# Performance work log

Hardware: AMD Instinct MI355X
Metric: run time of the kernel (lower is better)

## Reference

```python
import jax, jax.numpy as jnp
import numpy as np


def setup_inputs() -> dict:
    key = jax.random.key(0)
    B, T = 16384, 768
    inputs = jax.random.normal(key, (B, T, 2), dtype=jnp.float32)
    p = {"capacitance_x": 0.4, "capacitance_y": 0.4}
    for d in ["ax", "by", "xx", "xy", "yx", "yy"]:
        p[f"conductance_{d}"] = 0.001
        p[f"mean_{d}"] = 0.3
        p[f"std_{d}"] = 3.0
        p[f"pot_{d}"] = -1.0 if d in ("xy", "yx") else 1.0
    params = {k: jnp.full((1,), v, dtype=jnp.float32) for k, v in p.items()}
    return {"inputs": inputs, **params}


def reference(inputs, capacitance_x, capacitance_y,
              conductance_ax, mean_ax, std_ax, pot_ax,
              conductance_by, mean_by, std_by, pot_by,
              conductance_xx, mean_xx, std_xx, pot_xx,
              conductance_xy, mean_xy, std_xy, pot_xy,
              conductance_yx, mean_yx, std_yx, pot_yx,
              conductance_yy, mean_yy, std_yy, pot_yy):
    # inputs: [B, T, 2]; scan over T with carried state [B, 2]
    def syn(g, s, m, p, pre, post):
        # conductance * sigmoid(std*(pre-mean)) * (pot - post)
        return g * jax.nn.sigmoid(s * (pre - m)) * (p - post)

    def step(carry, inp):
        x, y = carry[:, :1], carry[:, 1:]          # [B,1] each
        a, b = inp[:, :1], inp[:, 1:]              # [B,1] each
        ix = (syn(conductance_ax, std_ax, mean_ax, pot_ax, a, x)
              + syn(conductance_xx, std_xx, mean_xx, pot_xx, x, x)
              + syn(conductance_yx, std_yx, mean_yx, pot_yx, y, x))
        iy = (syn(conductance_by, std_by, mean_by, pot_by, b, y)
              + syn(conductance_yy, std_yy, mean_yy, pot_yy, y, y)
              + syn(conductance_xy, std_xy, mean_xy, pot_xy, x, y))
        x = x + ix / capacitance_x
        y = y + iy / capacitance_y
        return jnp.concatenate([x, y], axis=-1), x

    B = inputs.shape[0]
    init = jnp.zeros((B, 2), dtype=inputs.dtype)
    _, ys = jax.lax.scan(step, init, jnp.swapaxes(inputs, 0, 1))  # ys: [T,B,1]
    return jnp.swapaxes(ys, 0, 1)  # [B,T,1]
```

## Files before the change

kernel.cpp:

```cpp
#include <hip/hip_runtime.h>

#define T_LEN 768
#define TC 64
#define NCH (T_LEN / TC)
#define RPB 32
#define RS  66
#define OS  66

struct Params { const float* p[27]; };

__device__ __forceinline__ float ex2(float x){ float r; asm("v_exp_f32 %0, %1":"=v"(r):"v"(x)); return r; }
__device__ __forceinline__ float frcp(float x){ return __builtin_amdgcn_rcpf(x); }
__device__ __forceinline__ float dpp_xor1(float x){
    return __int_as_float(__builtin_amdgcn_mov_dpp(__float_as_int(x),0xB1,0xF,0xF,true));
}
__device__ __forceinline__ float psig(float v, float k, float c){
    return frcp(1.0f + ex2(__builtin_fmaf(-k, v, c)));
}
__device__ __forceinline__ void wave_barrier(){
    asm volatile("s_waitcnt lgkmcnt(0)" ::: "memory");
    __builtin_amdgcn_s_barrier();
}

__global__ __launch_bounds__(192, 1) void cell_kernel(Params P, float* __restrict__ out) {
    __shared__ float r1buf[2][TC][RS];
    __shared__ float lds_o[2][TC][OS];

    const int tid = (int)threadIdx.x;
    const int r0  = (int)blockIdx.x * RPB;
    const int wv  = tid >> 6;
    const int l   = tid & 63;

    const float* __restrict__ inp = P.p[0];
    const float capx = P.p[1][0], capy = P.p[2][0];
    const float g_ax = P.p[3][0],  m_ax = P.p[4][0],  s_ax = P.p[5][0],  q_ax = P.p[6][0];
    const float g_by = P.p[7][0],  m_by = P.p[8][0],  s_by = P.p[9][0],  q_by = P.p[10][0];
    const float g_xx = P.p[11][0], m_xx = P.p[12][0], s_xx = P.p[13][0], q_xx = P.p[14][0];
    const float g_xy = P.p[15][0], m_xy = P.p[16][0], s_xy = P.p[17][0], q_xy = P.p[18][0];
    const float g_yx = P.p[19][0], m_yx = P.p[20][0], s_yx = P.p[21][0], q_yx = P.p[22][0];
    const float g_yy = P.p[23][0], m_yy = P.p[24][0], s_yy = P.p[25][0], q_yy = P.p[26][0];

    const float icx = 1.0f / capx, icy = 1.0f / capy;
    const float L2E  = 1.44269504088896340736f;
    const float LN2  = 0.69314718056f;
    const float mLN2 = -0.69314718056f;
    const float mHLN2 = -0.34657359028f;

    const float k1x = s_ax * L2E, c1x = k1x * m_ax;
    const float k1y = s_by * L2E, c1y = k1y * m_by;

    const bool share = (s_yx == s_yy) && (m_yx == m_yy) &&
                       (s_xy == s_xx) && (m_xy == m_xx) &&
                       (s_xx != 0.0f) && (s_yy != 0.0f) &&
                       (g_xx != 0.0f) && (g_yy != 0.0f);

    const float k2xp = s_xx * L2E, c2xp = k2xp * m_xx;
    const float G2xp = g_xx * icx;
    const float A2xp = g_xx * q_xx * icx;
    const float R2xp = __builtin_fmaf(G2xp, c2xp, -k2xp * A2xp);
    const float cv1 = share ? 1.0f / (G2xp * k2xp) : 1.0f;
    const float cv0 = share ? (c2xp / k2xp - R2xp * (1.0f / (G2xp * k2xp))) : 0.0f;

    const float4* __restrict__ in4 = (const float4*)inp;

    if (wv != 0) {
        const int p = wv - 1;
        float4 pinA[8], pinB[8];

        auto LOADP = [&](float4 (&pin)[8], int c) {
            #pragma unroll
            for (int k = 0; k < 8; ++k) { int idx = l + 64*(p*8 + k);
                int r_ = idx >> 5, q = idx & 31;
                pin[k] = in4[(size_t)(r0 + r_) * 384 + c * 32 + q]; }
        };
        auto SIGW = [&](float4 (&pin)[8], int buf) {
            #pragma unroll
            for (int k = 0; k < 8; ++k) { int idx = l + 64*(p*8 + k);
                int r_ = idx >> 5, q = idx & 31;
                float2 w0, w1;
                w0.x = psig(pin[k].x, k1x, c1x);
                w0.y = psig(pin[k].y, k1y, c1y);
                w1.x = psig(pin[k].z, k1x, c1x);
                w1.y = psig(pin[k].w, k1y, c1y);
                *(float2*)&r1buf[buf][2*q]    [2*r_] = w0;
                *(float2*)&r1buf[buf][2*q + 1][2*r_] = w1; }
        };
        auto DRAIN = [&](int c) {
            const int buf = c & 1;
            #pragma unroll
            for (int k = 0; k < 4; ++k) { int f = l + 64*(p*4 + k);
                int r_ = f >> 4, pq = f & 15;
                float4 o;
                o.x = __builtin_fmaf(lds_o[buf][4*pq + 0][2*r_], cv1, cv0);
                o.y = __builtin_fmaf(lds_o[buf][4*pq + 1][2*r_], cv1, cv0);
                o.z = __builtin_fmaf(lds_o[buf][4*pq + 2][2*r_], cv1, cv0);
                o.w = __builtin_fmaf(lds_o[buf][4*pq + 3][2*r_], cv1, cv0);
                *(float4*)&out[(size_t)(r0 + r_) * T_LEN + c * TC + 4*pq] = o; }
        };

        LOADP(pinA, 0);
        LOADP(pinB, 1);
        SIGW(pinA, 0);
        wave_barrier();
        for (int c = 0; c < NCH; ++c) {
            if (c + 2 < NCH) { if ((c & 1) == 0) LOADP(pinA, c + 2);
                               else              LOADP(pinB, c + 2); }
            if (c >= 1) DRAIN(c - 1);
            if (c + 1 < NCH) {
                if ((c & 1) == 0) SIGW(pinB, (c + 1) & 1);
                else              SIGW(pinA, (c + 1) & 1);
            }
            wave_barrier();
        }
        DRAIN(NCH - 1);
    } else {
        __builtin_amdgcn_s_setprio(1);

        const bool isX = (l & 1) == 0;
        const float k2r = (isX ? s_xx : s_yy) * L2E;
        const float c2r = k2r * (isX ? m_xx : m_yy);
        const float k3r = (isX ? s_xy : s_yx) * L2E;
        const float c3r = k3r * (isX ? m_xy : m_yx);
        const float icr = isX ? icx : icy;
        const float A1r = (isX ? g_ax * q_ax : g_by * q_by) * icr, G1r = (isX ? g_ax : g_by) * icr;
        const float A2r = (isX ? g_xx * q_xx : g_yy * q_yy) * icr, G2r = (isX ? g_xx : g_yy) * icr;
        const float A3r = (isX ? g_yx * q_yx : g_xy * q_xy) * icr, G3r = (isX ? g_yx : g_xy) * icr;

        const float R1 = __builtin_fmaf(G1r, c2r, -k2r * A1r);
        const float R2 = __builtin_fmaf(G2r, c2r, -k2r * A2r);
        const float R3 = __builtin_fmaf(G3r, c2r, -k2r * A3r);
        const float mG1 = -G1r, mG2 = -G2r, mG3 = -G3r;
        const float inv_mG2 = 1.0f / mG2;

        float h1 = __builtin_fmaf(mG1, c2r, R1);
        float h2 = __builtin_fmaf(mG2, c2r, R2);
        float h3 = __builtin_fmaf(mG3, c2r, R3);
        float v = 0.0f;

        wave_barrier();
        for (int c = 0; c < NCH; ++c) {
            const int buf = c & 1;
            float rr[TC];
            #pragma unroll
            for (int t = 0; t < TC; ++t) rr[t] = r1buf[buf][t][l];

            if (share) {
                float Wr  = (h2 - R2) * inv_mG2;
                float E   = ex2(Wr);
                float sg  = frcp(1.0f + E);
                float t1  = __builtin_fmaf(-sg, sg, sg);
                float cfac = mLN2 * t1;
                float w2  = __builtin_fmaf(LN2, sg, mHLN2);
                float hd2 = cfac * w2;
                float dl2p = 0.0f;
                float p1 = rr[0] * h1;
                #pragma unroll
                for (int t = 0; t < TC; ++t) {
                    float rp   = dpp_xor1(sg);
                    float s2mW = __builtin_fmaf(sg, h2, p1);
                    float dl   = __builtin_fmaf(rp, h3, s2mW);
                    float inner = __builtin_fmaf(hd2, dl2p, sg);
                    float sgn  = __builtin_fmaf(cfac, dl, inner);
                    dl2p = dl * dl;
                    h1 = __builtin_fmaf(mG1, dl, h1);
                    h2 = __builtin_fmaf(mG2, dl, h2);
                    h3 = __builtin_fmaf(mG3, dl, h3);
                    if (t + 1 < TC) p1 = rr[t + 1] * h1;
                    t1   = __builtin_fmaf(-sgn, sgn, sgn);
                    cfac = mLN2 * t1;
                    if ((t & 3) == 3) {
                        w2  = __builtin_fmaf(LN2, sgn, mHLN2);
                        hd2 = cfac * w2;
                    }
                    lds_o[buf][t][l] = h2;
                    sg = sgn;
                }
            } else {
                #pragma unroll
                for (int t = 0; t < TC; ++t) {
                    float s2 = psig(v, k2r, c2r);
                    float s3 = psig(v, k3r, c3r);
                    float rp = dpp_xor1(s3);
                    float u1 = __builtin_fmaf(-v, G1r, A1r);
                    float u2 = __builtin_fmaf(-v, G2r, A2r);
                    float u3 = __builtin_fmaf(-v, G3r, A3r);
                    v = __builtin_fmaf(rp, u3,
                        __builtin_fmaf(s2, u2,
                        __builtin_fmaf(rr[t], u1, v)));
                    lds_o[buf][t][l] = v;
                }
            }
            wave_barrier();
        }
    }
}

extern "C" void kernel_launch(void* const* d_in, const int* in_sizes, int n_in,
                              void* d_out, int out_size, void* d_ws, size_t ws_size,
                              hipStream_t stream) {
    (void)d_ws; (void)ws_size; (void)out_size; (void)n_in;
    Params P;
    for (int i = 0; i < 27; ++i) P.p[i] = (const float*)d_in[i];
    float* out = (float*)d_out;
    const int B = in_sizes[0] / (T_LEN * 2);
    dim3 grid(B / RPB);
    cell_kernel<<<grid, dim3(192), 0, stream>>>(P, out);
}
```

Baseline: 38.86 us.

## Interleave two independent recurrence chains per lane with 64 rows per block

Each lane of the recurrence wave now advances two independent rows (A and B) in lockstep, and each block covers 64 rows. The time chunk is halved so the LDS buffers keep the same footprint. Interleaving the chains is meant to hide the latency of the serial FMA/DPP/exp dependency chain through instruction-level parallelism. In exchange the grid has half as many blocks, the kernel runs twice as many chunk barriers, and register pressure rises.

```diff
diff --git a/kernel.cpp b/kernel.cpp
--- a/kernel.cpp
+++ b/kernel.cpp
@@ -1,11 +1,11 @@
 #include <hip/hip_runtime.h>
 
 #define T_LEN 768
-#define TC 64
+#define TC 32
 #define NCH (T_LEN / TC)
-#define RPB 32
-#define RS  66
-#define OS  66
+#define RPB 64
+#define RS  132
+#define OS  132
 
 struct Params { const float* p[27]; };
 
@@ -70,13 +70,13 @@
         auto LOADP = [&](float4 (&pin)[8], int c) {
             #pragma unroll
             for (int k = 0; k < 8; ++k) { int idx = l + 64*(p*8 + k);
-                int r_ = idx >> 5, q = idx & 31;
-                pin[k] = in4[(size_t)(r0 + r_) * 384 + c * 32 + q]; }
+                int r_ = idx >> 4, q = idx & 15;
+                pin[k] = in4[(size_t)(r0 + r_) * 384 + c * 16 + q]; }
         };
         auto SIGW = [&](float4 (&pin)[8], int buf) {
             #pragma unroll
             for (int k = 0; k < 8; ++k) { int idx = l + 64*(p*8 + k);
-                int r_ = idx >> 5, q = idx & 31;
+                int r_ = idx >> 4, q = idx & 15;
                 float2 w0, w1;
                 w0.x = psig(pin[k].x, k1x, c1x);
                 w0.y = psig(pin[k].y, k1y, c1y);
@@ -89,7 +89,7 @@
             const int buf = c & 1;
             #pragma unroll
             for (int k = 0; k < 4; ++k) { int f = l + 64*(p*4 + k);
-                int r_ = f >> 4, pq = f & 15;
+                int r_ = f >> 3, pq = f & 7;
                 float4 o;
                 o.x = __builtin_fmaf(lds_o[buf][4*pq + 0][2*r_], cv1, cv0);
                 o.y = __builtin_fmaf(lds_o[buf][4*pq + 1][2*r_], cv1, cv0);
@@ -132,62 +132,82 @@
         const float mG1 = -G1r, mG2 = -G2r, mG3 = -G3r;
         const float inv_mG2 = 1.0f / mG2;
 
-        float h1 = __builtin_fmaf(mG1, c2r, R1);
-        float h2 = __builtin_fmaf(mG2, c2r, R2);
-        float h3 = __builtin_fmaf(mG3, c2r, R3);
-        float v = 0.0f;
+        float h1A = __builtin_fmaf(mG1, c2r, R1), h1B = h1A;
+        float h2A = __builtin_fmaf(mG2, c2r, R2), h2B = h2A;
+        float h3A = __builtin_fmaf(mG3, c2r, R3), h3B = h3A;
+        float vA = 0.0f, vB = 0.0f;
 
         wave_barrier();
         for (int c = 0; c < NCH; ++c) {
             const int buf = c & 1;
-            float rr[TC];
-            #pragma unroll
-            for (int t = 0; t < TC; ++t) rr[t] = r1buf[buf][t][l];
-
+            float rrA[TC], rrB[TC];
+            #pragma unroll
+            for (int t = 0; t < TC; ++t) { rrA[t] = r1buf[buf][t][l];
+                                           rrB[t] = r1buf[buf][t][l + 64]; }
             if (share) {
-                float Wr  = (h2 - R2) * inv_mG2;
-                float E   = ex2(Wr);
-                float sg  = frcp(1.0f + E);
-                float t1  = __builtin_fmaf(-sg, sg, sg);
-                float cfac = mLN2 * t1;
-                float w2  = __builtin_fmaf(LN2, sg, mHLN2);
-                float hd2 = cfac * w2;
-                float dl2p = 0.0f;
-                float p1 = rr[0] * h1;
+                float WA = (h2A - R2) * inv_mG2;
+                float WB = (h2B - R2) * inv_mG2;
+                float sgA = frcp(1.0f + ex2(WA));
+                float sgB = frcp(1.0f + ex2(WB));
+                float t1A = __builtin_fmaf(-sgA, sgA, sgA);
+                float t1B = __builtin_fmaf(-sgB, sgB, sgB);
+                float cfA = mLN2 * t1A, cfB = mLN2 * t1B;
+                float hd2A = cfA * __builtin_fmaf(LN2, sgA, mHLN2);
+                float hd2B = cfB * __builtin_fmaf(LN2, sgB, mHLN2);
+                float dl2pA = 0.0f, dl2pB = 0.0f;
+                float p1A = rrA[0] * h1A, p1B = rrB[0] * h1B;
                 #pragma unroll
                 for (int t = 0; t < TC; ++t) {
-                    float rp   = dpp_xor1(sg);
-                    float s2mW = __builtin_fmaf(sg, h2, p1);
-                    float dl   = __builtin_fmaf(rp, h3, s2mW);
-                    float inner = __builtin_fmaf(hd2, dl2p, sg);
-                    float sgn  = __builtin_fmaf(cfac, dl, inner);
-                    dl2p = dl * dl;
-                    h1 = __builtin_fmaf(mG1, dl, h1);
-                    h2 = __builtin_fmaf(mG2, dl, h2);
-                    h3 = __builtin_fmaf(mG3, dl, h3);
-                    if (t + 1 < TC) p1 = rr[t + 1] * h1;
-                    t1   = __builtin_fmaf(-sgn, sgn, sgn);
-                    cfac = mLN2 * t1;
+                    float rpA = dpp_xor1(sgA);
+                    float rpB = dpp_xor1(sgB);
+                    float sA = __builtin_fmaf(sgA, h2A, p1A);
+                    float sB = __builtin_fmaf(sgB, h2B, p1B);
+                    float dlA = __builtin_fmaf(rpA, h3A, sA);
+                    float dlB = __builtin_fmaf(rpB, h3B, sB);
+                    float inA = __builtin_fmaf(hd2A, dl2pA, sgA);
+                    float inB = __builtin_fmaf(hd2B, dl2pB, sgB);
+                    float sgnA = __builtin_fmaf(cfA, dlA, inA);
+                    float sgnB = __builtin_fmaf(cfB, dlB, inB);
+                    dl2pA = dlA * dlA;  dl2pB = dlB * dlB;
+                    h1A = __builtin_fmaf(mG1, dlA, h1A);
+                    h2A = __builtin_fmaf(mG2, dlA, h2A);
+                    h3A = __builtin_fmaf(mG3, dlA, h3A);
+                    h1B = __builtin_fmaf(mG1, dlB, h1B);
+                    h2B = __builtin_fmaf(mG2, dlB, h2B);
+                    h3B = __builtin_fmaf(mG3, dlB, h3B);
+                    if (t + 1 < TC) { p1A = rrA[t+1] * h1A; p1B = rrB[t+1] * h1B; }
+                    t1A = __builtin_fmaf(-sgnA, sgnA, sgnA);
+                    t1B = __builtin_fmaf(-sgnB, sgnB, sgnB);
+                    cfA = mLN2 * t1A;  cfB = mLN2 * t1B;
                     if ((t & 3) == 3) {
-                        w2  = __builtin_fmaf(LN2, sgn, mHLN2);
-                        hd2 = cfac * w2;
+                        hd2A = cfA * __builtin_fmaf(LN2, sgnA, mHLN2);
+                        hd2B = cfB * __builtin_fmaf(LN2, sgnB, mHLN2);
                     }
-                    lds_o[buf][t][l] = h2;
-                    sg = sgn;
+                    lds_o[buf][t][l]      = h2A;
+                    lds_o[buf][t][l + 64] = h2B;
+                    sgA = sgnA;  sgB = sgnB;
                 }
             } else {
                 #pragma unroll
                 for (int t = 0; t < TC; ++t) {
-                    float s2 = psig(v, k2r, c2r);
-                    float s3 = psig(v, k3r, c3r);
-                    float rp = dpp_xor1(s3);
-                    float u1 = __builtin_fmaf(-v, G1r, A1r);
-                    float u2 = __builtin_fmaf(-v, G2r, A2r);
-                    float u3 = __builtin_fmaf(-v, G3r, A3r);
-                    v = __builtin_fmaf(rp, u3,
-                        __builtin_fmaf(s2, u2,
-                        __builtin_fmaf(rr[t], u1, v)));
-                    lds_o[buf][t][l] = v;
+                    float s2A = psig(vA, k2r, c2r);
+                    float s3A = psig(vA, k3r, c3r);
+                    float s2B = psig(vB, k2r, c2r);
+                    float s3B = psig(vB, k3r, c3r);
+                    float rpA = dpp_xor1(s3A);
+                    float rpB = dpp_xor1(s3B);
+                    float u1A = __builtin_fmaf(-vA, G1r, A1r);
+                    float u2A = __builtin_fmaf(-vA, G2r, A2r);
+                    float u3A = __builtin_fmaf(-vA, G3r, A3r);
+                    float u1B = __builtin_fmaf(-vB, G1r, A1r);
+                    float u2B = __builtin_fmaf(-vB, G2r, A2r);
+                    float u3B = __builtin_fmaf(-vB, G3r, A3r);
+                    vA = __builtin_fmaf(rpA, u3A,
+                         __builtin_fmaf(s2A, u2A, __builtin_fmaf(rrA[t], u1A, vA)));
+                    vB = __builtin_fmaf(rpB, u3B,
+                         __builtin_fmaf(s2B, u2B, __builtin_fmaf(rrB[t], u1B, vB)));
+                    lds_o[buf][t][l]      = vA;
+                    lds_o[buf][t][l + 64] = vB;
                 }
             }
             wave_barrier();
```

New measurement: 49.74 us. 1.28x slower.
